# Optimization experiments

Hardware: AMD Instinct MI355X
Metric: run time of the kernel (lower is better)

The kernel has to match this reference:

```python
import jax, jax.numpy as jnp
import numpy as np

B, L, T = 256, 1024, 128


def setup_inputs() -> dict:
    key = jax.random.key(0)
    k1, k2, k3, k4 = jax.random.split(key, 4)
    inputs = jax.random.normal(k1, (B, L, T), dtype=jnp.float32)
    lengths = jax.random.randint(k2, (B,), 1, L + 1, dtype=jnp.int32)
    tags = jax.random.randint(k3, (B, L), 0, T, dtype=jnp.int32)
    # learned CRF transition matrix (random_normal_initializer default stddev=0.05)
    transition_params = jax.random.normal(k4, (T, T), dtype=jnp.float32) * 0.05
    return {"inputs": inputs, "lengths": lengths, "tags": tags,
            "transition_params": transition_params}


def _crf_decode(x, trans, lengths):
    """Viterbi decode. x: [B,L,T], trans: [T,T], lengths: [B] -> tags [B,L] int32."""
    Bx, Lx, Tx = x.shape

    def fwd_step(state, inp):
        x_t, t = inp  # x_t: [B,T]
        scores = state[:, :, None] + trans[None]          # [B, T_prev, T_cur]
        bp = jnp.argmax(scores, axis=1).astype(jnp.int32)  # [B,T]
        new_state = jnp.max(scores, axis=1) + x_t           # [B,T]
        m = (t < lengths)[:, None]
        state = jnp.where(m, new_state, state)
        bp = jnp.where(m, bp, 0)
        return state, bp

    init = x[:, 0]                                          # [B,T]
    xs = (jnp.swapaxes(x[:, 1:], 0, 1), jnp.arange(1, Lx))
    state, bps = jax.lax.scan(fwd_step, init, xs)           # bps: [L-1,B,T]
    bps = jnp.concatenate([jnp.zeros((1, Bx, Tx), jnp.int32), bps], axis=0)  # bp[0] unused
    last_tag = jnp.argmax(state, axis=-1).astype(jnp.int32)  # [B] tag at position length-1

    def bwd_step(carry, inp):
        bp_t, t = inp
        emit = jnp.where(t < lengths, carry, 0)             # tags beyond length -> 0
        prev = jnp.take_along_axis(bp_t, carry[:, None], axis=1)[:, 0]
        carry = jnp.where((t > 0) & (t < lengths), prev, carry)
        return carry, emit

    _, tags_rev = jax.lax.scan(bwd_step, last_tag, (bps[::-1], jnp.arange(Lx)[::-1]))
    return jnp.swapaxes(tags_rev[::-1], 0, 1)               # [B,L]


def reference(inputs, lengths, tags, transition_params):
    # Decoder.call: tfa.text.crf_decode(inputs, transition_params, lengths)[0]
    return _crf_decode(inputs, transition_params, lengths)
```

## Files before the change

kernel.cpp:

```cpp
#include <hip/hip_runtime.h>

#define BB 256
#define LL 1024
#define TT 128
#define NTH 512
#define CH 64

typedef unsigned long long ull;

__device__ __forceinline__ void lds_barrier() {
    asm volatile("s_waitcnt lgkmcnt(0)\n\ts_barrier" ::);
}

struct FwdSmem {
    float state[TT];
    float pv[NTH];
    unsigned char tags[LL];
};

__global__ __launch_bounds__(NTH)
void viterbi_ws_kernel(const float* __restrict__ x,
                       const int* __restrict__ lengths,
                       const float* __restrict__ trans,
                       int* __restrict__ out,
                       float* __restrict__ ws) {
    __shared__ FwdSmem sm;
    extern __shared__ float dyn[];
    float* tT = dyn;
    float* bm = dyn + TT * TT;
    float* bx = bm + CH * TT;

    const int b   = blockIdx.x;
    const int tid = threadIdx.x;
    const int j   = tid & (TT - 1);
    const int q   = tid >> 7;

    int lenb = lengths[b];
    if (lenb < 1) lenb = 1;
    if (lenb > LL) lenb = LL;

    float tc[32];
    #pragma unroll
    for (int ii = 0; ii < 32; ++ii) {
        int r = q * 32 + ii;
        float v = trans[r * TT + j];
        tc[ii] = v;
        tT[j * TT + r] = v;
    }

    const float* xb  = x  + (size_t)b * LL * TT;
    float*       wsb = ws + (size_t)b * LL * TT;

    if (tid < TT) { float v = xb[tid]; sm.state[tid] = v; wsb[tid] = v; }

    float xv = 0.0f, xn = 0.0f;
    if (tid < TT && lenb > 1) xv = xb[TT + j];
    lds_barrier();

    for (int t = 1; t < lenb; ++t) {
        if (tid < TT) {
            int tn = (t + 1 < lenb) ? (t + 1) : (lenb - 1);
            xn = xb[tn * TT + j];
        }
        const float4* st4 = reinterpret_cast<const float4*>(sm.state + q * 32);
        float m0 = -3.4e38f, m1 = -3.4e38f, m2 = -3.4e38f, m3 = -3.4e38f;
        #pragma unroll
        for (int k = 0; k < 8; ++k) {
            float4 sv = st4[k];
            m0 = fmaxf(m0, sv.x + tc[4 * k + 0]);
            m1 = fmaxf(m1, sv.y + tc[4 * k + 1]);
            m2 = fmaxf(m2, sv.z + tc[4 * k + 2]);
            m3 = fmaxf(m3, sv.w + tc[4 * k + 3]);
        }
        sm.pv[tid] = fmaxf(fmaxf(m0, m1), fmaxf(m2, m3));
        lds_barrier();
        if (tid < TT) {
            float bv = fmaxf(fmaxf(sm.pv[j], sm.pv[j + 128]),
                             fmaxf(sm.pv[j + 256], sm.pv[j + 384]));
            wsb[t * TT + j] = bv;
            sm.state[j] = bv + xv;
            xv = xn;
        }
        lds_barrier();
    }

    __syncthreads();

    int c = 0; float mv = 0.0f;
    const int l = tid;
    if (tid < 64) {
        float s0 = sm.state[l], s1 = sm.state[l + 64];
        float mm = fmaxf(s0, s1);
        #pragma unroll
        for (int off = 1; off < 64; off <<= 1)
            mm = fmaxf(mm, __shfl_xor(mm, off));
        ull blo = __ballot(s0 == mm);
        if (blo) c = __ffsll(blo) - 1;
        else     c = 64 + __ffsll(__ballot(s1 == mm)) - 1;
        if (lenb > 1) mv = wsb[(lenb - 1) * TT + c];
    }

    int rhi = lenb - 2;
    while (rhi >= 0) {
        int r0 = rhi - (CH - 1); if (r0 < 0) r0 = 0;
        int nrows = rhi - r0 + 1;
        const float4* wm4 = reinterpret_cast<const float4*>(wsb + r0 * TT);
        const float4* wx4 = reinterpret_cast<const float4*>(xb  + r0 * TT);
        float4* bm4 = reinterpret_cast<float4*>(bm);
        float4* bx4 = reinterpret_cast<float4*>(bx);
        int n4 = nrows * (TT / 4);
        for (int i4 = tid; i4 < n4; i4 += NTH) {
            bm4[i4] = wm4[i4];
            float4 v = wx4[i4];
            if (r0 == 0 && i4 < TT / 4) { v.x = 0.f; v.y = 0.f; v.z = 0.f; v.w = 0.f; }
            bx4[i4] = v;
        }
        lds_barrier();
        if (tid < 64) {
            for (int t = r0 + nrows; t >= r0 + 1; --t) {
                int row = (t - 1 - r0) * TT;
                float slo = (bm[row + l]      + bx[row + l])      + tT[c * TT + l];
                float shi = (bm[row + 64 + l] + bx[row + 64 + l]) + tT[c * TT + 64 + l];
                ull blo = __ballot(slo == mv);
                int nc;
                if (blo) nc = __ffsll(blo) - 1;
                else     nc = 64 + __ffsll(__ballot(shi == mv)) - 1;
                if (l == 0) sm.tags[t] = (unsigned char)c;
                c = nc;
                mv = bm[row + c];
            }
        }
        lds_barrier();
        rhi = r0 - 1;
    }
    if (tid == 0) sm.tags[0] = (unsigned char)c;
    lds_barrier();

    int* outb = out + (size_t)b * LL;
    for (int t = tid; t < LL; t += NTH)
        outb[t] = (t < lenb) ? (int)sm.tags[t] : 0;
}

struct SmallSmem {
    float state[TT];
    float pv[NTH];
    int   pi[NTH];
    unsigned char tags[LL];
};

__global__ __launch_bounds__(NTH)
void viterbi_kernel(const float* __restrict__ x,
                    const int* __restrict__ lengths,
                    const float* __restrict__ trans,
                    int* __restrict__ out) {
    __shared__ SmallSmem sm;
    extern __shared__ unsigned char bp[];

    const int b   = blockIdx.x;
    const int tid = threadIdx.x;
    const int j   = tid & (TT - 1);
    const int q   = tid >> 7;

    int lenb = lengths[b];
    if (lenb < 1) lenb = 1;
    if (lenb > LL) lenb = LL;

    float tc[32];
    #pragma unroll
    for (int ii = 0; ii < 32; ++ii)
        tc[ii] = trans[(q * 32 + ii) * TT + j];

    const float* xb = x + (size_t)b * LL * TT;
    if (tid < TT) sm.state[tid] = xb[tid];

    float xv_cur = 0.0f, xv_next = 0.0f;
    if (tid < TT && lenb > 1) xv_cur = xb[TT + j];
    lds_barrier();

    for (int t = 1; t < lenb; ++t) {
        if (tid < TT) {
            int tn = (t + 1 < lenb) ? (t + 1) : (lenb - 1);
            xv_next = xb[tn * TT + j];
        }
        float best0 = -3.4e38f, best1 = -3.4e38f, best2 = -3.4e38f, best3 = -3.4e38f;
        int   bi0 = 0, bi1 = 1, bi2 = 2, bi3 = 3;
        const float4* st4 = reinterpret_cast<const float4*>(sm.state + q * 32);
        #pragma unroll
        for (int k = 0; k < 8; ++k) {
            float4 sv = st4[k];
            float s0 = sv.x + tc[4 * k + 0];
            float s1 = sv.y + tc[4 * k + 1];
            float s2 = sv.z + tc[4 * k + 2];
            float s3 = sv.w + tc[4 * k + 3];
            if (s0 > best0) { best0 = s0; bi0 = 4 * k + 0; }
            if (s1 > best1) { best1 = s1; bi1 = 4 * k + 1; }
            if (s2 > best2) { best2 = s2; bi2 = 4 * k + 2; }
            if (s3 > best3) { best3 = s3; bi3 = 4 * k + 3; }
        }
        float bb = best0; int bi = bi0;
        if (best1 > bb || (best1 == bb && bi1 < bi)) { bb = best1; bi = bi1; }
        if (best2 > bb || (best2 == bb && bi2 < bi)) { bb = best2; bi = bi2; }
        if (best3 > bb || (best3 == bb && bi3 < bi)) { bb = best3; bi = bi3; }
        sm.pv[tid] = bb;
        sm.pi[tid] = bi + q * 32;
        lds_barrier();

        if (tid < TT) {
            float bv = sm.pv[j];       int ix = sm.pi[j];
            float v1 = sm.pv[j + 128]; int i1 = sm.pi[j + 128];
            float v2 = sm.pv[j + 256]; int i2 = sm.pi[j + 256];
            float v3 = sm.pv[j + 384]; int i3 = sm.pi[j + 384];
            if (v1 > bv) { bv = v1; ix = i1; }
            if (v2 > bv) { bv = v2; ix = i2; }
            if (v3 > bv) { bv = v3; ix = i3; }
            sm.state[j] = bv + xv_cur;
            bp[t * TT + j] = (unsigned char)ix;
            xv_cur = xv_next;
        }
        lds_barrier();
    }

    if (tid == 0) {
        float bv = sm.state[0]; int ix = 0;
        for (int i = 1; i < TT; ++i) {
            float v = sm.state[i];
            if (v > bv) { bv = v; ix = i; }
        }
        int carry = ix;
        for (int t = lenb - 1; t >= 1; --t) {
            sm.tags[t] = (unsigned char)carry;
            carry = bp[t * TT + carry];
        }
        sm.tags[0] = (unsigned char)carry;
    }
    lds_barrier();

    int* outb = out + (size_t)b * LL;
    for (int t = tid; t < LL; t += NTH)
        outb[t] = (t < lenb) ? (int)sm.tags[t] : 0;
}

extern "C" void kernel_launch(void* const* d_in, const int* in_sizes, int n_in,
                              void* d_out, int out_size, void* d_ws, size_t ws_size,
                              hipStream_t stream) {
    const float* x       = (const float*)d_in[0];
    const int*   lengths = (const int*)d_in[1];
    const float* trans   = (const float*)d_in[3];
    int*         out     = (int*)d_out;

    const size_t ws_needed = (size_t)BB * LL * TT * sizeof(float);

    if (d_ws != nullptr && ws_size >= ws_needed) {
        const int dyn = (TT * TT + 2 * CH * TT) * (int)sizeof(float);
        hipFuncSetAttribute((const void*)&viterbi_ws_kernel,
                            hipFuncAttributeMaxDynamicSharedMemorySize, dyn);
        viterbi_ws_kernel<<<BB, NTH, dyn, stream>>>(x, lengths, trans, out,
                                                    (float*)d_ws);
    } else {
        const int dyn = LL * TT;
        hipFuncSetAttribute((const void*)&viterbi_kernel,
                            hipFuncAttributeMaxDynamicSharedMemorySize, dyn);
        viterbi_kernel<<<BB, NTH, dyn, stream>>>(x, lengths, trans, out);
    }
}
```

Before: 776.1 us.

## Reduce Viterbi partial maxima with DPP and double-buffer state to drop a barrier

The forward Viterbi recurrence now assigns the four partial maxima of each tag to adjacent lanes, so they can be combined with DPP cross-lane swizzles instead of a shared-memory exchange. The state vector is double-buffered in LDS, which leaves one barrier per timestep instead of two. State rows are padded to avoid bank conflicts, and the transposed transition table gets a padded stride of 129. The aim is to shorten the serial per-step latency chain. The cost is a more complex index mapping and slightly more LDS.

```diff
diff --git a/kernel.cpp b/kernel.cpp
--- a/kernel.cpp
+++ b/kernel.cpp
@@ -5,6 +5,7 @@
 #define TT 128
 #define NTH 512
 #define CH 64
+#define TTP 129
 
 typedef unsigned long long ull;
 
@@ -12,9 +13,17 @@
     asm volatile("s_waitcnt lgkmcnt(0)\n\ts_barrier" ::);
 }
 
+template<int CTRL>
+__device__ __forceinline__ float dpp_f(float v) {
+    int r = __builtin_amdgcn_update_dpp(__float_as_int(v), __float_as_int(v),
+                                        CTRL, 0xF, 0xF, false);
+    return __int_as_float(r);
+}
+
+#define SP(i) ((i) + (((i) >> 5) << 2))
+
 struct FwdSmem {
-    float state[TT];
-    float pv[NTH];
+    float st[2][144];
     unsigned char tags[LL];
 };
 
@@ -27,13 +36,13 @@
     __shared__ FwdSmem sm;
     extern __shared__ float dyn[];
     float* tT = dyn;
-    float* bm = dyn + TT * TT;
+    float* bm = dyn + TTP * TT;
     float* bx = bm + CH * TT;
 
     const int b   = blockIdx.x;
     const int tid = threadIdx.x;
-    const int j   = tid & (TT - 1);
-    const int q   = tid >> 7;
+    const int j   = tid >> 2;
+    const int q   = tid & 3;
 
     int lenb = lengths[b];
     if (lenb < 1) lenb = 1;
@@ -41,28 +50,37 @@
 
     float tc[32];
     #pragma unroll
-    for (int ii = 0; ii < 32; ++ii) {
-        int r = q * 32 + ii;
-        float v = trans[r * TT + j];
-        tc[ii] = v;
-        tT[j * TT + r] = v;
+    for (int ii = 0; ii < 32; ++ii)
+        tc[ii] = trans[(q * 32 + ii) * TT + j];
+
+    {
+        const int jj = tid & (TT - 1);
+        const int qq = tid >> 7;
+        #pragma unroll
+        for (int ii = 0; ii < 32; ++ii) {
+            int r = qq * 32 + ii;
+            tT[jj * TTP + r] = trans[r * TT + jj];
+        }
     }
 
     const float* xb  = x  + (size_t)b * LL * TT;
     float*       wsb = ws + (size_t)b * LL * TT;
 
-    if (tid < TT) { float v = xb[tid]; sm.state[tid] = v; wsb[tid] = v; }
-
-    float xv = 0.0f, xn = 0.0f;
-    if (tid < TT && lenb > 1) xv = xb[TT + j];
-    lds_barrier();
-
+    if (tid < TT) { float v = xb[tid]; sm.st[0][SP(tid)] = v; wsb[tid] = v; }
+
+    float xv = 0.0f;
+    if (q == 0 && lenb > 1) xv = xb[TT + j];
+    lds_barrier();
+
+    int p = 0;
     for (int t = 1; t < lenb; ++t) {
-        if (tid < TT) {
+        float xn = 0.0f;
+        if (q == 0) {
             int tn = (t + 1 < lenb) ? (t + 1) : (lenb - 1);
             xn = xb[tn * TT + j];
         }
-        const float4* st4 = reinterpret_cast<const float4*>(sm.state + q * 32);
+
+        const float4* st4 = reinterpret_cast<const float4*>(&sm.st[p][q * 36]);
         float m0 = -3.4e38f, m1 = -3.4e38f, m2 = -3.4e38f, m3 = -3.4e38f;
         #pragma unroll
         for (int k = 0; k < 8; ++k) {
@@ -72,15 +90,16 @@
             m2 = fmaxf(m2, sv.z + tc[4 * k + 2]);
             m3 = fmaxf(m3, sv.w + tc[4 * k + 3]);
         }
-        sm.pv[tid] = fmaxf(fmaxf(m0, m1), fmaxf(m2, m3));
-        lds_barrier();
-        if (tid < TT) {
-            float bv = fmaxf(fmaxf(sm.pv[j], sm.pv[j + 128]),
-                             fmaxf(sm.pv[j + 256], sm.pv[j + 384]));
-            wsb[t * TT + j] = bv;
-            sm.state[j] = bv + xv;
+        float bb = fmaxf(fmaxf(m0, m1), fmaxf(m2, m3));
+        bb = fmaxf(bb, dpp_f<0xB1>(bb));
+        bb = fmaxf(bb, dpp_f<0x4E>(bb));
+
+        if (q == 0) {
+            wsb[t * TT + j] = bb;
+            sm.st[p ^ 1][SP(j)] = bb + xv;
             xv = xn;
         }
+        p ^= 1;
         lds_barrier();
     }
 
@@ -89,7 +108,7 @@
     int c = 0; float mv = 0.0f;
     const int l = tid;
     if (tid < 64) {
-        float s0 = sm.state[l], s1 = sm.state[l + 64];
+        float s0 = sm.st[p][SP(l)], s1 = sm.st[p][SP(l + 64)];
         float mm = fmaxf(s0, s1);
         #pragma unroll
         for (int off = 1; off < 64; off <<= 1)
@@ -119,8 +138,8 @@
         if (tid < 64) {
             for (int t = r0 + nrows; t >= r0 + 1; --t) {
                 int row = (t - 1 - r0) * TT;
-                float slo = (bm[row + l]      + bx[row + l])      + tT[c * TT + l];
-                float shi = (bm[row + 64 + l] + bx[row + 64 + l]) + tT[c * TT + 64 + l];
+                float slo = (bm[row + l]      + bx[row + l])      + tT[c * TTP + l];
+                float shi = (bm[row + 64 + l] + bx[row + 64 + l]) + tT[c * TTP + 64 + l];
                 ull blo = __ballot(slo == mv);
                 int nc;
                 if (blo) nc = __ffsll(blo) - 1;
@@ -251,7 +270,7 @@
     const size_t ws_needed = (size_t)BB * LL * TT * sizeof(float);
 
     if (d_ws != nullptr && ws_size >= ws_needed) {
-        const int dyn = (TT * TT + 2 * CH * TT) * (int)sizeof(float);
+        const int dyn = (TTP * TT + 2 * CH * TT) * (int)sizeof(float);
         hipFuncSetAttribute((const void*)&viterbi_ws_kernel,
                             hipFuncAttributeMaxDynamicSharedMemorySize, dyn);
         viterbi_ws_kernel<<<BB, NTH, dyn, stream>>>(x, lengths, trans, out,
```

Result: slower. 825.8 us (+6.4%).
